# Kernel optimization log

Hardware: AMD Instinct MI355X
Metric: run time of the kernel (lower is better)

## Reference

```python
import jax, jax.numpy as jnp
import numpy as np


def setup_inputs() -> dict:
    key = jax.random.key(0)
    k1, k2 = jax.random.split(key)
    TOKENS, IN, OUT = 32768, 1024, 1024
    x = jax.random.normal(k1, (TOKENS, IN), dtype=jnp.float32)
    # weight init: uniform(-1, 1) over [out_features, in_features]
    weight = jax.random.uniform(k2, (OUT, IN), dtype=jnp.float32, minval=-1.0, maxval=1.0)
    b = jnp.zeros((OUT,), dtype=jnp.float32)
    return {"x": x, "weight": weight, "b": b}


def reference(x, weight, b):
    # ternary quantization: sign() zeros out exact zeros; mask keeps nonzeros
    sign = jnp.sign(weight)
    mask = (weight != 0).astype(x.dtype)
    w_q = sign * mask  # [out, in], values in {-1, 0, 1}
    # F.linear: x @ w_q.T + b
    return jnp.einsum("ti,oi->to", x, w_q) + b
```

## Files before the change

### kernel.cpp

```cpp
#include <hip/hip_runtime.h>
#include <hip/hip_bf16.h>


typedef int   i32x4 __attribute__((ext_vector_type(4)));
typedef float f32x4 __attribute__((ext_vector_type(4)));

#define BM 128
#define BN 128
#define BK 64

__device__ __forceinline__ void async16(const void* gptr, void* lptr) {
    __builtin_amdgcn_global_load_lds(
        (const __attribute__((address_space(1))) unsigned int*)gptr,
        (__attribute__((address_space(3))) unsigned int*)lptr,
        16, 0, 0);
}

__device__ __forceinline__ int clamp127(int v) {
    v = v > 127 ? 127 : v;
    v = v < -127 ? -127 : v;
    return v;
}

__device__ __forceinline__ int pack4(int a, int b, int c, int d) {
    return (a & 255) | ((b & 255) << 8) | ((c & 255) << 16) | ((d & 255) << 24);
}

__device__ __forceinline__ int sgnb(float v) {
    return (v > 0.0f) ? 1 : ((v < 0.0f) ? -1 : 0);
}


__global__ __launch_bounds__(256)
void quant_pre(const float* __restrict__ x, const float* __restrict__ w,
               signed char* __restrict__ xq, signed char* __restrict__ wq,
               float* __restrict__ scales, int M, int K, long nw, int xblocks) {
    const int tid = threadIdx.x;

    if ((int)blockIdx.x >= xblocks) {
        long i = ((long)(blockIdx.x - xblocks) * 256 + tid) * 8;
        if (i + 8 > nw) return;
        const float4* p = (const float4*)(w + i);
        float4 a = p[0];
        float4 b = p[1];
        int lo = pack4(sgnb(a.x), sgnb(a.y), sgnb(a.z), sgnb(a.w));
        int hi = pack4(sgnb(b.x), sgnb(b.y), sgnb(b.z), sgnb(b.w));
        int2 v; v.x = lo; v.y = hi;
        *(int2*)(wq + i) = v;
        return;
    }

    const int wv   = tid >> 6;
    const int lane = tid & 63;
    const int row  = blockIdx.x * 4 + wv;
    if (row >= M) return;

    const float* xr = x + (long)row * K;
    const int chunks = K >> 8;
    float4 v[8];
    float m = 0.0f;
#pragma unroll
    for (int q = 0; q < 8; ++q) {
        if (q >= chunks) break;
        v[q] = *(const float4*)(xr + q * 256 + lane * 4);
        m = fmaxf(m, fmaxf(fmaxf(fabsf(v[q].x), fabsf(v[q].y)),
                           fmaxf(fabsf(v[q].z), fabsf(v[q].w))));
    }
#pragma unroll
    for (int off = 32; off > 0; off >>= 1)
        m = fmaxf(m, __shfl_xor(m, off, 64));

    const float inv = (m > 0.0f) ? (127.0f / m) : 0.0f;
    int* qr = (int*)(xq + (long)row * K);
#pragma unroll
    for (int q = 0; q < 8; ++q) {
        if (q >= chunks) break;
        int a = clamp127(__float2int_rn(v[q].x * inv));
        int b = clamp127(__float2int_rn(v[q].y * inv));
        int c = clamp127(__float2int_rn(v[q].z * inv));
        int d = clamp127(__float2int_rn(v[q].w * inv));
        qr[q * 64 + lane] = pack4(a, b, c, d);
    }
    if (lane == 0) scales[row] = m * (1.0f / 127.0f);
}


__global__ __launch_bounds__(256)
void gemm_i8(const signed char* __restrict__ A, const signed char* __restrict__ B,
             const float* __restrict__ scales, const float* __restrict__ bias,
             float* __restrict__ C, int M, int N, int K, int swz) {
    __shared__ __align__(16) signed char sA[BM * BK];
    __shared__ __align__(16) signed char sB[BN * BK];

    const int tid  = threadIdx.x;
    const int lane = tid & 63;
    const int wave = tid >> 6;

    const int gn = N / BN;
    int mt, nt;
    if (swz) {
        const int b    = blockIdx.x;
        const int xcd  = b & 7;
        const int rest = b >> 3;
        nt = rest % gn;
        mt = (rest / gn) * 8 + xcd;
    } else {
        nt = blockIdx.x % gn;
        mt = blockIdx.x / gn;
    }
    const int bm = mt * BM;
    const int bn = nt * BN;

    const int wrow = (wave >> 1) * 64;
    const int wcol = (wave & 1) * 64;
    const int quad = lane >> 4;
    const int l16  = lane & 15;

    i32x4 acc[4][4] = {};

    const int row0  = tid >> 2;
    const int col16 = (tid & 3) * 16;
    const signed char* pa0 = A + (long)(bm + row0) * K + col16;
    const signed char* pa1 = pa0 + (long)64 * K;
    const signed char* pb0 = B + (long)(bn + row0) * K + col16;
    const signed char* pb1 = pb0 + (long)64 * K;

    for (int k0 = 0; k0 < K; k0 += BK) {
        async16(pa0 + k0, (char*)sA + tid * 16);
        async16(pa1 + k0, (char*)sA + (256 + tid) * 16);
        async16(pb0 + k0, (char*)sB + tid * 16);
        async16(pb1 + k0, (char*)sB + (256 + tid) * 16);
        __syncthreads();

        i32x4 af[4], bfr[4];
#pragma unroll
        for (int i = 0; i < 4; ++i) {
            af[i]  = *(const i32x4*)&sA[(wrow + i * 16 + l16) * BK + quad * 16];
            bfr[i] = *(const i32x4*)&sB[(wcol + i * 16 + l16) * BK + quad * 16];
        }
#pragma unroll
        for (int i = 0; i < 4; ++i)
#pragma unroll
            for (int j = 0; j < 4; ++j)
                acc[i][j] = __builtin_amdgcn_mfma_i32_16x16x64_i8(af[i], bfr[j], acc[i][j], 0, 0, 0);

        __syncthreads();
    }

#pragma unroll
    for (int j = 0; j < 4; ++j) {
        const int col = bn + wcol + j * 16 + l16;
        const float bv = bias[col];
#pragma unroll
        for (int i = 0; i < 4; ++i) {
            const int rbase = bm + wrow + i * 16 + quad * 4;
#pragma unroll
            for (int r = 0; r < 4; ++r) {
                const int row = rbase + r;
                C[(long)row * N + col] = (float)acc[i][j][r] * scales[row] + bv;
            }
        }
    }
}


__device__ __forceinline__ float signf(float v) {
    return (v > 0.0f) ? 1.0f : ((v < 0.0f) ? -1.0f : 0.0f);
}

__global__ void fallback_kernel(const float* __restrict__ x, const float* __restrict__ w,
                                const float* __restrict__ b, float* __restrict__ out,
                                int M, int N, int K) {
    long o = (long)blockIdx.x * blockDim.x + threadIdx.x;
    if (o >= (long)M * N) return;
    int t = (int)(o / N);
    int n = (int)(o % N);
    const float* xr = x + (long)t * K;
    const float* wr = w + (long)n * K;
    float s = 0.0f;
    for (int k = 0; k < K; ++k) s += xr[k] * signf(wr[k]);
    out[o] = s + b[n];
}


extern "C" void kernel_launch(void* const* d_in, const int* in_sizes, int n_in,
                              void* d_out, int out_size, void* d_ws, size_t ws_size,
                              hipStream_t stream) {
    const float* x = (const float*)d_in[0];
    const float* w = (const float*)d_in[1];
    const float* b = (const float*)d_in[2];
    float* out = (float*)d_out;

    const int N = in_sizes[2];
    const int K = in_sizes[1] / N;
    const int M = in_sizes[0] / K;

    const long nx = (long)M * K;
    const long nw = (long)N * K;
    const size_t need = (size_t)nx + (size_t)nw + (size_t)M * 4 + 64;

    const bool fast = (M % BM == 0) && (N % BN == 0) && (K % BK == 0) &&
                      (K % 256 == 0) && (K <= 2048) && (nw % 2048 == 0) &&
                      (ws_size >= need);

    if (!fast) {
        long total = (long)M * N;
        int blocks = (int)((total + 255) / 256);
        fallback_kernel<<<blocks, 256, 0, stream>>>(x, w, b, out, M, N, K);
        return;
    }

    signed char* xq = (signed char*)d_ws;
    signed char* wq = xq + nx;
    float* scales   = (float*)(wq + nw);

    const int xblocks = M / 4;
    const int wblocks = (int)(nw / 2048);
    quant_pre<<<xblocks + wblocks, 256, 0, stream>>>(x, w, xq, wq, scales, M, K, nw, xblocks);

    const int gm = M / BM, gn = N / BN;
    const int swz = (gm % 8 == 0) ? 1 : 0;
    gemm_i8<<<gm * gn, 256, 0, stream>>>(xq, wq, scales, b, out, M, N, K, swz);
}
```

Before: 287.3 us.

## Double K tile, XOR-swizzle LDS layout, and vectorize epilogue via swapped MFMA operands

Raises BK from 64 to 128 so each barrier pair covers two MFMA k-steps, halving the synchronization count per tile. The global-to-LDS copy and the fragment reads use an XOR swizzle on 16-byte columns to avoid LDS bank conflicts. MFMA operands are swapped so each lane holds four consecutive output columns, which lets the epilogue issue 16-byte vector stores and bias loads instead of scalar strided stores. Doubling the LDS footprint to 32KB may reduce occupancy.

Measured after the change: 279.6 us. -2.7%, faster.

```diff
diff --git a/kernel.cpp b/kernel.cpp
--- a/kernel.cpp
+++ b/kernel.cpp
@@ -7,7 +7,7 @@
 
 #define BM 128
 #define BN 128
-#define BK 64
+#define BK 128
 
 __device__ __forceinline__ void async16(const void* gptr, void* lptr) {
     __builtin_amdgcn_global_load_lds(
@@ -118,47 +118,58 @@
 
     i32x4 acc[4][4] = {};
 
-    const int row0  = tid >> 2;
-    const int col16 = (tid & 3) * 16;
-    const signed char* pa0 = A + (long)(bm + row0) * K + col16;
-    const signed char* pa1 = pa0 + (long)64 * K;
-    const signed char* pb0 = B + (long)(bn + row0) * K + col16;
-    const signed char* pb1 = pb0 + (long)64 * K;
+    const int srow = tid >> 3;
+    const int scol = 16 * ((tid & 7) ^ (srow & 7));
+    const signed char* pa = A + (long)(bm + srow) * K + scol;
+    const signed char* pb = B + (long)(bn + srow) * K + scol;
+    const long rstride = (long)32 * K;
+
+    const int rswz  = (l16 & 7) << 4;
+    const int offk0 = (quad * 16) ^ rswz;
+    const int offk1 = (64 + quad * 16) ^ rswz;
 
     for (int k0 = 0; k0 < K; k0 += BK) {
-        async16(pa0 + k0, (char*)sA + tid * 16);
-        async16(pa1 + k0, (char*)sA + (256 + tid) * 16);
-        async16(pb0 + k0, (char*)sB + tid * 16);
-        async16(pb1 + k0, (char*)sB + (256 + tid) * 16);
+#pragma unroll
+        for (int p = 0; p < 4; ++p) {
+            async16(pa + p * rstride + k0, (char*)sA + p * 4096 + tid * 16);
+            async16(pb + p * rstride + k0, (char*)sB + p * 4096 + tid * 16);
+        }
         __syncthreads();
 
-        i32x4 af[4], bfr[4];
-#pragma unroll
-        for (int i = 0; i < 4; ++i) {
-            af[i]  = *(const i32x4*)&sA[(wrow + i * 16 + l16) * BK + quad * 16];
-            bfr[i] = *(const i32x4*)&sB[(wcol + i * 16 + l16) * BK + quad * 16];
+#pragma unroll
+        for (int kk = 0; kk < 2; ++kk) {
+            const int off = kk ? offk1 : offk0;
+            i32x4 af[4], bfr[4];
+#pragma unroll
+            for (int i = 0; i < 4; ++i) {
+                af[i]  = *(const i32x4*)&sA[(wrow + i * 16 + l16) * BK + off];
+                bfr[i] = *(const i32x4*)&sB[(wcol + i * 16 + l16) * BK + off];
+            }
+#pragma unroll
+            for (int i = 0; i < 4; ++i)
+#pragma unroll
+                for (int j = 0; j < 4; ++j)
+                    acc[i][j] = __builtin_amdgcn_mfma_i32_16x16x64_i8(bfr[j], af[i], acc[i][j], 0, 0, 0);
         }
-#pragma unroll
-        for (int i = 0; i < 4; ++i)
-#pragma unroll
-            for (int j = 0; j < 4; ++j)
-                acc[i][j] = __builtin_amdgcn_mfma_i32_16x16x64_i8(af[i], bfr[j], acc[i][j], 0, 0, 0);
 
         __syncthreads();
     }
 
 #pragma unroll
-    for (int j = 0; j < 4; ++j) {
-        const int col = bn + wcol + j * 16 + l16;
-        const float bv = bias[col];
-#pragma unroll
-        for (int i = 0; i < 4; ++i) {
-            const int rbase = bm + wrow + i * 16 + quad * 4;
-#pragma unroll
-            for (int r = 0; r < 4; ++r) {
-                const int row = rbase + r;
-                C[(long)row * N + col] = (float)acc[i][j][r] * scales[row] + bv;
-            }
+    for (int i = 0; i < 4; ++i) {
+        const int row = bm + wrow + i * 16 + l16;
+        const float sc = scales[row];
+        float* cr = C + (long)row * N;
+#pragma unroll
+        for (int j = 0; j < 4; ++j) {
+            const int n0 = bn + wcol + j * 16 + quad * 4;
+            const f32x4 bv = *(const f32x4*)&bias[n0];
+            f32x4 o;
+            o[0] = (float)acc[i][j][0] * sc + bv[0];
+            o[1] = (float)acc[i][j][1] * sc + bv[1];
+            o[2] = (float)acc[i][j][2] * sc + bv[2];
+            o[3] = (float)acc[i][j][3] * sc + bv[3];
+            *(f32x4*)&cr[n0] = o;
         }
     }
 }
```

## Double-buffer LDS, swizzle layout, switch to 32x32 MFMA with vectorized stores

Applied to the files above, without the earlier changes.

The int8 GEMM gets double-buffered LDS staging, so the async global-to-LDS loads for the next K tile overlap with MFMA compute on the current one, and it drops one barrier per iteration. Shared memory uses an XOR-swizzled 128-byte-row layout to avoid bank conflicts, and the inner product moves from 16x16x64 to 32x32x32 int8 MFMA. Operands are swapped so each lane holds contiguous output columns, which allows 16-byte vectorized stores of C. It doubles LDS use and assumes K/BK is even and at least 2, which the dispatch check does not enforce.

Result: no change. 289.3 us (+0.7%).

```diff
diff --git a/kernel.cpp b/kernel.cpp
--- a/kernel.cpp
+++ b/kernel.cpp
@@ -2,8 +2,9 @@
 #include <hip/hip_bf16.h>
 
 
-typedef int   i32x4 __attribute__((ext_vector_type(4)));
-typedef float f32x4 __attribute__((ext_vector_type(4)));
+typedef int   i32x4  __attribute__((ext_vector_type(4)));
+typedef int   i32x16 __attribute__((ext_vector_type(16)));
+typedef float f32x4  __attribute__((ext_vector_type(4)));
 
 #define BM 128
 #define BN 128
@@ -89,8 +90,8 @@
 void gemm_i8(const signed char* __restrict__ A, const signed char* __restrict__ B,
              const float* __restrict__ scales, const float* __restrict__ bias,
              float* __restrict__ C, int M, int N, int K, int swz) {
-    __shared__ __align__(16) signed char sA[BM * BK];
-    __shared__ __align__(16) signed char sB[BN * BK];
+    __shared__ __align__(16) signed char sA[2][64 * 128];
+    __shared__ __align__(16) signed char sB[2][64 * 128];
 
     const int tid  = threadIdx.x;
     const int lane = tid & 63;
@@ -113,54 +114,113 @@
 
     const int wrow = (wave >> 1) * 64;
     const int wcol = (wave & 1) * 64;
-    const int quad = lane >> 4;
-    const int l16  = lane & 15;
-
-    i32x4 acc[4][4] = {};
-
-    const int row0  = tid >> 2;
-    const int col16 = (tid & 3) * 16;
-    const signed char* pa0 = A + (long)(bm + row0) * K + col16;
-    const signed char* pa1 = pa0 + (long)64 * K;
-    const signed char* pb0 = B + (long)(bn + row0) * K + col16;
-    const signed char* pb1 = pb0 + (long)64 * K;
-
-    for (int k0 = 0; k0 < K; k0 += BK) {
-        async16(pa0 + k0, (char*)sA + tid * 16);
-        async16(pa1 + k0, (char*)sA + (256 + tid) * 16);
-        async16(pb0 + k0, (char*)sB + tid * 16);
-        async16(pb1 + k0, (char*)sB + (256 + tid) * 16);
+    const int l31  = lane & 31;
+    const int ksel = lane >> 5;
+    const int halfA = wave >> 1;
+    const int halfB = wave & 1;
+
+    const int s0 = tid, s1 = tid + 256;
+    const int lr0 = s0 >> 3, lr1 = s1 >> 3;
+    const int cc0 = (s0 & 7) ^ (lr0 & 7);
+    const int cc1 = (s1 & 7) ^ (lr1 & 7);
+    const long goA0 = (long)(bm + (cc0 >> 2) * 64 + lr0) * K + (cc0 & 3) * 16;
+    const long goA1 = (long)(bm + (cc1 >> 2) * 64 + lr1) * K + (cc1 & 3) * 16;
+    const long goB0 = (long)(bn + (cc0 >> 2) * 64 + lr0) * K + (cc0 & 3) * 16;
+    const long goB1 = (long)(bn + (cc1 >> 2) * 64 + lr1) * K + (cc1 & 3) * 16;
+    const int d0 = s0 * 16, d1 = s1 * 16;
+
+#define STAGE(buf, k0)                                             \
+    do {                                                           \
+        async16(A + goA0 + (k0), (char*)sA[buf] + d0);             \
+        async16(A + goA1 + (k0), (char*)sA[buf] + d1);             \
+        async16(B + goB0 + (k0), (char*)sB[buf] + d0);             \
+        async16(B + goB1 + (k0), (char*)sB[buf] + d1);             \
+    } while (0)
+
+    const int rsw = (l31 & 7) << 4;
+    const int ccA0 = (halfA * 4 + 0 * 2 + ksel) << 4;
+    const int ccA1 = (halfA * 4 + 1 * 2 + ksel) << 4;
+    const int ccB0 = (halfB * 4 + 0 * 2 + ksel) << 4;
+    const int ccB1 = (halfB * 4 + 1 * 2 + ksel) << 4;
+    const int rA0 = l31 * 128;
+    const int rA1 = (32 + l31) * 128;
+    const int oA00 = rA0 + (ccA0 ^ rsw);
+    const int oA01 = rA0 + (ccA1 ^ rsw);
+    const int oA10 = rA1 + (ccA0 ^ rsw);
+    const int oA11 = rA1 + (ccA1 ^ rsw);
+    const int oB00 = rA0 + (ccB0 ^ rsw);
+    const int oB01 = rA0 + (ccB1 ^ rsw);
+    const int oB10 = rA1 + (ccB0 ^ rsw);
+    const int oB11 = rA1 + (ccB1 ^ rsw);
+
+    i32x16 acc00 = {}, acc01 = {}, acc10 = {}, acc11 = {};
+
+#define COMPUTE(buf)                                                          \
+    do {                                                                      \
+        const signed char* a_ = sA[buf];                                      \
+        const signed char* b_ = sB[buf];                                      \
+        i32x4 a0 = *(const i32x4*)(a_ + oA00);                                \
+        i32x4 a1 = *(const i32x4*)(a_ + oA10);                                \
+        i32x4 b0 = *(const i32x4*)(b_ + oB00);                                \
+        i32x4 b1 = *(const i32x4*)(b_ + oB10);                                \
+        acc00 = __builtin_amdgcn_mfma_i32_32x32x32_i8(b0, a0, acc00, 0, 0, 0);\
+        acc01 = __builtin_amdgcn_mfma_i32_32x32x32_i8(b1, a0, acc01, 0, 0, 0);\
+        acc10 = __builtin_amdgcn_mfma_i32_32x32x32_i8(b0, a1, acc10, 0, 0, 0);\
+        acc11 = __builtin_amdgcn_mfma_i32_32x32x32_i8(b1, a1, acc11, 0, 0, 0);\
+        a0 = *(const i32x4*)(a_ + oA01);                                      \
+        a1 = *(const i32x4*)(a_ + oA11);                                      \
+        b0 = *(const i32x4*)(b_ + oB01);                                      \
+        b1 = *(const i32x4*)(b_ + oB11);                                      \
+        acc00 = __builtin_amdgcn_mfma_i32_32x32x32_i8(b0, a0, acc00, 0, 0, 0);\
+        acc01 = __builtin_amdgcn_mfma_i32_32x32x32_i8(b1, a0, acc01, 0, 0, 0);\
+        acc10 = __builtin_amdgcn_mfma_i32_32x32x32_i8(b0, a1, acc10, 0, 0, 0);\
+        acc11 = __builtin_amdgcn_mfma_i32_32x32x32_i8(b1, a1, acc11, 0, 0, 0);\
+    } while (0)
+
+    const int NT = K / BK;
+    STAGE(0, 0);
+    __syncthreads();
+    int k0 = 0;
+    for (int t = 0; t < NT / 2 - 1; ++t) {
+        STAGE(1, k0 + BK);
+        COMPUTE(0);
         __syncthreads();
-
-        i32x4 af[4], bfr[4];
-#pragma unroll
-        for (int i = 0; i < 4; ++i) {
-            af[i]  = *(const i32x4*)&sA[(wrow + i * 16 + l16) * BK + quad * 16];
-            bfr[i] = *(const i32x4*)&sB[(wcol + i * 16 + l16) * BK + quad * 16];
-        }
-#pragma unroll
-        for (int i = 0; i < 4; ++i)
-#pragma unroll
-            for (int j = 0; j < 4; ++j)
-                acc[i][j] = __builtin_amdgcn_mfma_i32_16x16x64_i8(af[i], bfr[j], acc[i][j], 0, 0, 0);
-
+        STAGE(0, k0 + 2 * BK);
+        COMPUTE(1);
         __syncthreads();
-    }
-
-#pragma unroll
-    for (int j = 0; j < 4; ++j) {
-        const int col = bn + wcol + j * 16 + l16;
-        const float bv = bias[col];
-#pragma unroll
-        for (int i = 0; i < 4; ++i) {
-            const int rbase = bm + wrow + i * 16 + quad * 4;
-#pragma unroll
-            for (int r = 0; r < 4; ++r) {
-                const int row = rbase + r;
-                C[(long)row * N + col] = (float)acc[i][j][r] * scales[row] + bv;
-            }
-        }
-    }
+        k0 += 2 * BK;
+    }
+    STAGE(1, k0 + BK);
+    COMPUTE(0);
+    __syncthreads();
+    COMPUTE(1);
+
+#undef STAGE
+#undef COMPUTE
+
+#define STORE_FRAG(accv, i, j)                                          \
+    do {                                                                \
+        const int row = bm + wrow + (i) * 32 + l31;                     \
+        const float sc = scales[row];                                   \
+        float* cr = C + (long)row * N + bn + wcol + (j) * 32;           \
+        _Pragma("unroll")                                               \
+        for (int g = 0; g < 4; ++g) {                                   \
+            const int n0 = g * 8 + ksel * 4;                            \
+            const f32x4 bv = *(const f32x4*)&bias[bn + wcol + (j) * 32 + n0]; \
+            f32x4 o;                                                    \
+            o[0] = (float)(accv)[4 * g + 0] * sc + bv[0];               \
+            o[1] = (float)(accv)[4 * g + 1] * sc + bv[1];               \
+            o[2] = (float)(accv)[4 * g + 2] * sc + bv[2];               \
+            o[3] = (float)(accv)[4 * g + 3] * sc + bv[3];               \
+            *(f32x4*)&cr[n0] = o;                                       \
+        }                                                               \
+    } while (0)
+
+    STORE_FRAG(acc00, 0, 0);
+    STORE_FRAG(acc01, 0, 1);
+    STORE_FRAG(acc10, 1, 0);
+    STORE_FRAG(acc11, 1, 1);
+#undef STORE_FRAG
 }
 
 
```

## Fuse activation quantization into a row-resident int8 GEMM with 32x32 MFMA

Applied to the files above, without the earlier changes.

Removes the separate x-quantization pass. Each block now quantizes its 128 rows of x straight into a 128 KB XOR-swizzled LDS tile and keeps them resident while it sweeps every N tile. Weight tiles are double-buffered through async global-to-LDS loads, the MFMA moves from 16x16x64 to 32x32x32 int8, and outputs go out as vectorized float4 stores. This drops the int8 activation round trip through global memory and one launch, at the cost of a single 4-wave block per CU with very large LDS use, a grid of only M/128 blocks, and a fast path hard-wired to K==1024.

After: 367.3 us. +27.9%, slower.

```diff
diff --git a/kernel.cpp b/kernel.cpp
--- a/kernel.cpp
+++ b/kernel.cpp
@@ -1,9 +1,9 @@
 #include <hip/hip_runtime.h>
-#include <hip/hip_bf16.h>
-
-
-typedef int   i32x4 __attribute__((ext_vector_type(4)));
-typedef float f32x4 __attribute__((ext_vector_type(4)));
+
+
+typedef int   i32x4  __attribute__((ext_vector_type(4)));
+typedef int   i32x16 __attribute__((ext_vector_type(16)));
+typedef float f32x4  __attribute__((ext_vector_type(4)));
 
 #define BM 128
 #define BN 128
@@ -30,137 +30,187 @@
     return (v > 0.0f) ? 1 : ((v < 0.0f) ? -1 : 0);
 }
 
+__device__ __forceinline__ float max4(float4 v) {
+    return fmaxf(fmaxf(fabsf(v.x), fabsf(v.y)), fmaxf(fabsf(v.z), fabsf(v.w)));
+}
+
+__device__ __forceinline__ int q4(float4 v, float inv) {
+    return pack4(clamp127(__float2int_rn(v.x * inv)),
+                 clamp127(__float2int_rn(v.y * inv)),
+                 clamp127(__float2int_rn(v.z * inv)),
+                 clamp127(__float2int_rn(v.w * inv)));
+}
+
 
 __global__ __launch_bounds__(256)
-void quant_pre(const float* __restrict__ x, const float* __restrict__ w,
-               signed char* __restrict__ xq, signed char* __restrict__ wq,
-               float* __restrict__ scales, int M, int K, long nw, int xblocks) {
-    const int tid = threadIdx.x;
-
-    if ((int)blockIdx.x >= xblocks) {
-        long i = ((long)(blockIdx.x - xblocks) * 256 + tid) * 8;
-        if (i + 8 > nw) return;
-        const float4* p = (const float4*)(w + i);
-        float4 a = p[0];
-        float4 b = p[1];
-        int lo = pack4(sgnb(a.x), sgnb(a.y), sgnb(a.z), sgnb(a.w));
-        int hi = pack4(sgnb(b.x), sgnb(b.y), sgnb(b.z), sgnb(b.w));
-        int2 v; v.x = lo; v.y = hi;
-        *(int2*)(wq + i) = v;
-        return;
-    }
-
-    const int wv   = tid >> 6;
-    const int lane = tid & 63;
-    const int row  = blockIdx.x * 4 + wv;
-    if (row >= M) return;
-
-    const float* xr = x + (long)row * K;
-    const int chunks = K >> 8;
-    float4 v[8];
-    float m = 0.0f;
-#pragma unroll
-    for (int q = 0; q < 8; ++q) {
-        if (q >= chunks) break;
-        v[q] = *(const float4*)(xr + q * 256 + lane * 4);
-        m = fmaxf(m, fmaxf(fmaxf(fabsf(v[q].x), fabsf(v[q].y)),
-                           fmaxf(fabsf(v[q].z), fabsf(v[q].w))));
-    }
-#pragma unroll
-    for (int off = 32; off > 0; off >>= 1)
-        m = fmaxf(m, __shfl_xor(m, off, 64));
-
-    const float inv = (m > 0.0f) ? (127.0f / m) : 0.0f;
-    int* qr = (int*)(xq + (long)row * K);
-#pragma unroll
-    for (int q = 0; q < 8; ++q) {
-        if (q >= chunks) break;
-        int a = clamp127(__float2int_rn(v[q].x * inv));
-        int b = clamp127(__float2int_rn(v[q].y * inv));
-        int c = clamp127(__float2int_rn(v[q].z * inv));
-        int d = clamp127(__float2int_rn(v[q].w * inv));
-        qr[q * 64 + lane] = pack4(a, b, c, d);
-    }
-    if (lane == 0) scales[row] = m * (1.0f / 127.0f);
+void wsign_kernel(const float* __restrict__ w, signed char* __restrict__ wq,
+                  long nw) {
+    long i = ((long)blockIdx.x * 256 + threadIdx.x) * 8;
+    if (i + 8 > nw) return;
+    const float4* p = (const float4*)(w + i);
+    float4 a = p[0];
+    float4 b = p[1];
+    int lo = pack4(sgnb(a.x), sgnb(a.y), sgnb(a.z), sgnb(a.w));
+    int hi = pack4(sgnb(b.x), sgnb(b.y), sgnb(b.z), sgnb(b.w));
+    int2 v; v.x = lo; v.y = hi;
+    *(int2*)(wq + i) = v;
 }
 
 
 __global__ __launch_bounds__(256)
-void gemm_i8(const signed char* __restrict__ A, const signed char* __restrict__ B,
-             const float* __restrict__ scales, const float* __restrict__ bias,
-             float* __restrict__ C, int M, int N, int K, int swz) {
-    __shared__ __align__(16) signed char sA[BM * BK];
-    __shared__ __align__(16) signed char sB[BN * BK];
+void gemm_fused(const float* __restrict__ x, const signed char* __restrict__ B,
+                const float* __restrict__ bias, float* __restrict__ C,
+                int N, int K) {
+    __shared__ __align__(16) signed char sA[BM * 1024];
+    __shared__ __align__(16) signed char sB[2 * 64 * 128];
+    __shared__ float s_scales[BM];
 
     const int tid  = threadIdx.x;
     const int lane = tid & 63;
     const int wave = tid >> 6;
-
-    const int gn = N / BN;
-    int mt, nt;
-    if (swz) {
-        const int b    = blockIdx.x;
-        const int xcd  = b & 7;
-        const int rest = b >> 3;
-        nt = rest % gn;
-        mt = (rest / gn) * 8 + xcd;
-    } else {
-        nt = blockIdx.x % gn;
-        mt = blockIdx.x / gn;
-    }
-    const int bm = mt * BM;
-    const int bn = nt * BN;
-
-    const int wrow = (wave >> 1) * 64;
-    const int wcol = (wave & 1) * 64;
-    const int quad = lane >> 4;
-    const int l16  = lane & 15;
-
-    i32x4 acc[4][4] = {};
-
-    const int row0  = tid >> 2;
-    const int col16 = (tid & 3) * 16;
-    const signed char* pa0 = A + (long)(bm + row0) * K + col16;
-    const signed char* pa1 = pa0 + (long)64 * K;
-    const signed char* pb0 = B + (long)(bn + row0) * K + col16;
-    const signed char* pb1 = pb0 + (long)64 * K;
-
-    for (int k0 = 0; k0 < K; k0 += BK) {
-        async16(pa0 + k0, (char*)sA + tid * 16);
-        async16(pa1 + k0, (char*)sA + (256 + tid) * 16);
-        async16(pb0 + k0, (char*)sB + tid * 16);
-        async16(pb1 + k0, (char*)sB + (256 + tid) * 16);
-        __syncthreads();
-
-        i32x4 af[4], bfr[4];
+    const int bm   = blockIdx.x * BM;
+
+    const int s0 = tid, s1 = tid + 256;
+    const int lr0 = s0 >> 3, lr1 = s1 >> 3;
+    const int cc0 = (s0 & 7) ^ (lr0 & 7);
+    const int cc1 = (s1 & 7) ^ (lr1 & 7);
+    const long offB0 = (long)((cc0 >> 2) * 64 + lr0) * K + (cc0 & 3) * 16;
+    const long offB1 = (long)((cc1 >> 2) * 64 + lr1) * K + (cc1 & 3) * 16;
+    const int d0 = s0 * 16, d1 = s1 * 16;
+
+#define STAGEB(bb, s2)                                                   \
+    do {                                                                 \
+        const int nt2 = (s2) >> 4, ks2 = (s2) & 15;                      \
+        const signed char* bp = B + (long)nt2 * 128 * K + ks2 * 64;      \
+        async16(bp + offB0, (char*)sB + (bb) * 8192 + d0);               \
+        async16(bp + offB1, (char*)sB + (bb) * 8192 + d1);               \
+    } while (0)
+
+    STAGEB(0, 0);
+
+    {
+        const int rbase = wave * 32;
+#pragma unroll 4
+        for (int rr = 0; rr < 32; rr += 2) {
+            const int ra = rbase + rr, rb = ra + 1;
+            const float4* pa = (const float4*)(x + (long)(bm + ra) * K + lane * 16);
+            const float4* pb = (const float4*)(x + (long)(bm + rb) * K + lane * 16);
+            float4 a0 = pa[0], a1 = pa[1], a2 = pa[2], a3 = pa[3];
+            float4 b0 = pb[0], b1 = pb[1], b2 = pb[2], b3 = pb[3];
+            float ma = fmaxf(fmaxf(max4(a0), max4(a1)), fmaxf(max4(a2), max4(a3)));
+            float mb = fmaxf(fmaxf(max4(b0), max4(b1)), fmaxf(max4(b2), max4(b3)));
 #pragma unroll
-        for (int i = 0; i < 4; ++i) {
-            af[i]  = *(const i32x4*)&sA[(wrow + i * 16 + l16) * BK + quad * 16];
-            bfr[i] = *(const i32x4*)&sB[(wcol + i * 16 + l16) * BK + quad * 16];
-        }
-#pragma unroll
-        for (int i = 0; i < 4; ++i)
-#pragma unroll
-            for (int j = 0; j < 4; ++j)
-                acc[i][j] = __builtin_amdgcn_mfma_i32_16x16x64_i8(af[i], bfr[j], acc[i][j], 0, 0, 0);
-
-        __syncthreads();
-    }
-
-#pragma unroll
-    for (int j = 0; j < 4; ++j) {
-        const int col = bn + wcol + j * 16 + l16;
-        const float bv = bias[col];
-#pragma unroll
-        for (int i = 0; i < 4; ++i) {
-            const int rbase = bm + wrow + i * 16 + quad * 4;
-#pragma unroll
-            for (int r = 0; r < 4; ++r) {
-                const int row = rbase + r;
-                C[(long)row * N + col] = (float)acc[i][j][r] * scales[row] + bv;
+            for (int off = 32; off > 0; off >>= 1) {
+                ma = fmaxf(ma, __shfl_xor(ma, off, 64));
+                mb = fmaxf(mb, __shfl_xor(mb, off, 64));
+            }
+            const float ia = (ma > 0.0f) ? (127.0f / ma) : 0.0f;
+            const float ib = (mb > 0.0f) ? (127.0f / mb) : 0.0f;
+            i32x4 qa, qb;
+            qa[0] = q4(a0, ia); qa[1] = q4(a1, ia); qa[2] = q4(a2, ia); qa[3] = q4(a3, ia);
+            qb[0] = q4(b0, ib); qb[1] = q4(b1, ib); qb[2] = q4(b2, ib); qb[3] = q4(b3, ib);
+            *(i32x4*)&sA[ra * 1024 + ((lane ^ (ra & 15)) << 4)] = qa;
+            *(i32x4*)&sA[rb * 1024 + ((lane ^ (rb & 15)) << 4)] = qb;
+            if (lane == 0) {
+                s_scales[ra] = ma * (1.0f / 127.0f);
+                s_scales[rb] = mb * (1.0f / 127.0f);
             }
         }
     }
+    __syncthreads();
+
+    const int wrow = (wave >> 1) * 64;
+    const int wcol = (wave & 1) * 64;
+    const int l31  = lane & 31;
+    const int ksel = lane >> 5;
+    const int halfB = wave & 1;
+    const int lx   = l31 & 15;
+
+    const int rowA0 = (wrow + l31) * 1024;
+    const int rowA1 = rowA0 + 32 * 1024;
+
+    const int rsw  = (l31 & 7) << 4;
+    const int ccB0 = (halfB * 4 + 0 + ksel) << 4;
+    const int ccB1 = (halfB * 4 + 2 + ksel) << 4;
+    const int rB0  = l31 * 128;
+    const int rB1  = (32 + l31) * 128;
+    const int oB00 = rB0 + (ccB0 ^ rsw);
+    const int oB01 = rB0 + (ccB1 ^ rsw);
+    const int oB10 = rB1 + (ccB0 ^ rsw);
+    const int oB11 = rB1 + (ccB1 ^ rsw);
+
+    const i32x16 zz = {};
+    i32x16 acc00 = zz, acc01 = zz, acc10 = zz, acc11 = zz;
+
+#define COMPUTE(ks, bb)                                                       \
+    do {                                                                      \
+        const signed char* b_ = sB + (bb) * 8192;                             \
+        const int c0 = (ks) * 4 + ksel;                                       \
+        const int c1 = c0 + 2;                                                \
+        i32x4 a0 = *(const i32x4*)&sA[rowA0 + ((c0 ^ lx) << 4)];              \
+        i32x4 a1 = *(const i32x4*)&sA[rowA1 + ((c0 ^ lx) << 4)];              \
+        i32x4 b0 = *(const i32x4*)(b_ + oB00);                                \
+        i32x4 b1 = *(const i32x4*)(b_ + oB10);                                \
+        acc00 = __builtin_amdgcn_mfma_i32_32x32x32_i8(b0, a0, acc00, 0, 0, 0);\
+        acc01 = __builtin_amdgcn_mfma_i32_32x32x32_i8(b1, a0, acc01, 0, 0, 0);\
+        acc10 = __builtin_amdgcn_mfma_i32_32x32x32_i8(b0, a1, acc10, 0, 0, 0);\
+        acc11 = __builtin_amdgcn_mfma_i32_32x32x32_i8(b1, a1, acc11, 0, 0, 0);\
+        a0 = *(const i32x4*)&sA[rowA0 + ((c1 ^ lx) << 4)];                    \
+        a1 = *(const i32x4*)&sA[rowA1 + ((c1 ^ lx) << 4)];                    \
+        b0 = *(const i32x4*)(b_ + oB01);                                      \
+        b1 = *(const i32x4*)(b_ + oB11);                                      \
+        acc00 = __builtin_amdgcn_mfma_i32_32x32x32_i8(b0, a0, acc00, 0, 0, 0);\
+        acc01 = __builtin_amdgcn_mfma_i32_32x32x32_i8(b1, a0, acc01, 0, 0, 0);\
+        acc10 = __builtin_amdgcn_mfma_i32_32x32x32_i8(b0, a1, acc10, 0, 0, 0);\
+        acc11 = __builtin_amdgcn_mfma_i32_32x32x32_i8(b1, a1, acc11, 0, 0, 0);\
+    } while (0)
+
+#define STORE_FRAG(accv, i, j, nt)                                            \
+    do {                                                                      \
+        const int row = bm + wrow + (i) * 32 + l31;                           \
+        const float sc = s_scales[wrow + (i) * 32 + l31];                     \
+        const int cb = (nt) * 128 + wcol + (j) * 32;                          \
+        float* cr = C + (long)row * N + cb;                                   \
+        _Pragma("unroll")                                                     \
+        for (int g = 0; g < 4; ++g) {                                         \
+            const int n0 = g * 8 + ksel * 4;                                  \
+            const f32x4 bv = *(const f32x4*)&bias[cb + n0];                   \
+            f32x4 o;                                                          \
+            o[0] = (float)(accv)[4 * g + 0] * sc + bv[0];                     \
+            o[1] = (float)(accv)[4 * g + 1] * sc + bv[1];                     \
+            o[2] = (float)(accv)[4 * g + 2] * sc + bv[2];                     \
+            o[3] = (float)(accv)[4 * g + 3] * sc + bv[3];                     \
+            *(f32x4*)&cr[n0] = o;                                             \
+        }                                                                     \
+    } while (0)
+
+    const int total = (N / BN) * (K / BK);
+    for (int s = 0; s < total; ++s) {
+        const int bb = s & 1;
+        if (s + 1 < total) {
+            STAGEB(bb ^ 1, s + 1);
+            asm volatile("s_waitcnt vmcnt(2)" ::: "memory");
+        } else {
+            asm volatile("s_waitcnt vmcnt(0)" ::: "memory");
+        }
+        __builtin_amdgcn_sched_barrier(0);
+        __builtin_amdgcn_s_barrier();
+        __builtin_amdgcn_sched_barrier(0);
+        COMPUTE(s & 15, bb);
+        if ((s & 15) == 15) {
+            const int nt = s >> 4;
+            STORE_FRAG(acc00, 0, 0, nt);
+            STORE_FRAG(acc01, 0, 1, nt);
+            STORE_FRAG(acc10, 1, 0, nt);
+            STORE_FRAG(acc11, 1, 1, nt);
+            acc00 = zz; acc01 = zz; acc10 = zz; acc11 = zz;
+        }
+        __builtin_amdgcn_s_barrier();
+    }
+
+#undef STAGEB
+#undef COMPUTE
+#undef STORE_FRAG
 }
 
 
@@ -195,13 +245,10 @@
     const int K = in_sizes[1] / N;
     const int M = in_sizes[0] / K;
 
-    const long nx = (long)M * K;
     const long nw = (long)N * K;
-    const size_t need = (size_t)nx + (size_t)nw + (size_t)M * 4 + 64;
-
-    const bool fast = (M % BM == 0) && (N % BN == 0) && (K % BK == 0) &&
-                      (K % 256 == 0) && (K <= 2048) && (nw % 2048 == 0) &&
-                      (ws_size >= need);
+
+    const bool fast = (K == 1024) && (M % BM == 0) && (N % BN == 0) &&
+                      (nw % 2048 == 0) && (ws_size >= (size_t)nw);
 
     if (!fast) {
         long total = (long)M * N;
@@ -210,15 +257,8 @@
         return;
     }
 
-    signed char* xq = (signed char*)d_ws;
-    signed char* wq = xq + nx;
-    float* scales   = (float*)(wq + nw);
-
-    const int xblocks = M / 4;
-    const int wblocks = (int)(nw / 2048);
-    quant_pre<<<xblocks + wblocks, 256, 0, stream>>>(x, w, xq, wq, scales, M, K, nw, xblocks);
-
-    const int gm = M / BM, gn = N / BN;
-    const int swz = (gm % 8 == 0) ? 1 : 0;
-    gemm_i8<<<gm * gn, 256, 0, stream>>>(xq, wq, scales, b, out, M, N, K, swz);
-}
+    signed char* wq = (signed char*)d_ws;
+
+    wsign_kernel<<<(int)(nw / 2048), 256, 0, stream>>>(w, wq, nw);
+    gemm_fused<<<M / BM, 256, 0, stream>>>(x, wq, b, out, N, K);
+}
```
